# Performance work log

Hardware: AMD Instinct MI355X
Metric: run time of the kernel (lower is better)

The kernel has to match this reference:

```python
import jax, jax.numpy as jnp
import numpy as np

BINS = 10
LOSS_WEIGHT = 1.0
EDGE_TOP = 1.0 + 1e-6  # edges[-1] += 1e-6 in the torch module


def setup_inputs() -> dict:
    key = jax.random.key(0)
    k1, k2, k3 = jax.random.split(key, 3)
    shape = (32, 1048576)
    # pred: sigmoid probabilities in [0, 1)
    pred = jax.random.uniform(k1, shape, dtype=jnp.float32)
    target = (jax.random.uniform(k2, shape) < 0.3).astype(jnp.float32)
    label_weight = (jax.random.uniform(k3, shape) < 0.95).astype(jnp.float32)
    return {"pred": pred, "target": target, "label_weight": label_weight}


def reference(pred, target, label_weight):
    p = pred.reshape(-1)
    t = target.reshape(-1).astype(p.dtype)
    lw = label_weight.reshape(-1).astype(p.dtype)

    I = jnp.sum(p * t)                       # intersection
    S = jnp.sum(p) + jnp.sum(t)              # denominator of Dice

    # gradient norm proxy: |2I/S * pred.detach() - target| (no grad flows through g)
    g = jax.lax.stop_gradient(jnp.abs(2.0 * I / S * p - t))

    valid = lw > 0
    tot = jnp.maximum(jnp.sum(valid.astype(p.dtype)), 1.0)

    # bin assignment: edges are i/bins for i=0..bins, with edges[-1] bumped by 1e-6,
    # so g in [i/bins, (i+1)/bins) -> bin i, and g in [1, 1+1e-6) -> bin bins-1.
    in_range = valid & (g < EDGE_TOP)
    bin_idx = jnp.clip(jnp.floor(g * BINS).astype(jnp.int32), 0, BINS - 1)

    # one-pass histogram of valid, in-range elements
    counts = jnp.zeros(BINS, dtype=p.dtype).at[bin_idx].add(in_range.astype(p.dtype))
    n_nonempty = jnp.sum(counts > 0).astype(p.dtype)

    # weight = tot / num_in_bin for elements in a non-empty bin, else 0; then /n
    per_elem = jnp.where(in_range, tot / jnp.maximum(counts[bin_idx], 1.0), 0.0)
    weights = per_elem / jnp.maximum(n_nonempty, 1.0)

    loss = 1.0 - jnp.sum(2.0 * p * t * weights) / S
    return loss * LOSS_WEIGHT
```

## Files before the change

### kernel.cpp

```cpp
#include <hip/hip_runtime.h>


constexpr int BINS   = 10;
constexpr int K      = 4;
constexpr int CH     = 256 * K;
constexpr int BLOCKS = 2048;
constexpr int OFF1   = 64;
constexpr int OFF2   = 16448;

__global__ __launch_bounds__(256) void k_reduce1(const float4* __restrict__ p,
                                                 const float4* __restrict__ t,
                                                 float* __restrict__ ws,
                                                 int n4, int n) {
    const int tid   = threadIdx.x;
    const int nfull = n4 / CH;
    float sI = 0.f, sP = 0.f, sT = 0.f;

    for (int c = blockIdx.x; c < nfull; c += gridDim.x) {
        const int base = c * CH + tid;
        float4 pv[K], tv[K];
#pragma unroll
        for (int k = 0; k < K; ++k) pv[k] = p[base + k * 256];
#pragma unroll
        for (int k = 0; k < K; ++k) tv[k] = t[base + k * 256];
#pragma unroll
        for (int k = 0; k < K; ++k) {
            sI += pv[k].x * tv[k].x + pv[k].y * tv[k].y + pv[k].z * tv[k].z + pv[k].w * tv[k].w;
            sP += pv[k].x + pv[k].y + pv[k].z + pv[k].w;
            sT += tv[k].x + tv[k].y + tv[k].z + tv[k].w;
        }
    }
    if (blockIdx.x == 0) {
        for (int i = nfull * CH + tid; i < n4; i += 256) {
            float4 pv = p[i], tv = t[i];
            sI += pv.x * tv.x + pv.y * tv.y + pv.z * tv.z + pv.w * tv.w;
            sP += pv.x + pv.y + pv.z + pv.w;
            sT += tv.x + tv.y + tv.z + tv.w;
        }
        if (tid == 0) {
            const float* pf = (const float*)p;
            const float* tf = (const float*)t;
            for (int i = n4 * 4; i < n; ++i) { sI += pf[i] * tf[i]; sP += pf[i]; sT += tf[i]; }
        }
    }
#pragma unroll
    for (int o = 32; o > 0; o >>= 1) {
        sI += __shfl_down(sI, o);
        sP += __shfl_down(sP, o);
        sT += __shfl_down(sT, o);
    }
    __shared__ float rI[4], rP[4], rT[4];
    int wave = tid >> 6, lane = tid & 63;
    if (lane == 0) { rI[wave] = sI; rP[wave] = sP; rT[wave] = sT; }
    __syncthreads();
    if (tid == 0) {
        float* o = &ws[OFF1 + blockIdx.x * 4];
        o[0] = rI[0] + rI[1] + rI[2] + rI[3];
        o[1] = rP[0] + rP[1] + rP[2] + rP[3];
        o[2] = rT[0] + rT[1] + rT[2] + rT[3];
    }
}

__global__ __launch_bounds__(256) void k_mid(float* __restrict__ ws, int nb1) {
    const float4* pws = (const float4*)&ws[OFF1];
    float aI = 0.f, aP = 0.f, aT = 0.f;
    for (int b = threadIdx.x; b < nb1; b += 256) {
        float4 v = pws[b];
        aI += v.x; aP += v.y; aT += v.z;
    }
    __shared__ float red[256 * 5];
    float* mine = &red[threadIdx.x * 5];
    mine[0] = aI; mine[1] = aP; mine[2] = aT;
    __syncthreads();
    int tid = threadIdx.x;
    if (tid < 3) {
        float s = 0.f;
        for (int i = 0; i < 256; ++i) s += red[i * 5 + tid];
        red[tid] = s;
    }
    __syncthreads();
    if (tid == 0) {
        float I = red[0];
        float S = red[1] + red[2];
        ws[0] = 2.f * I / S;
        ws[1] = S;
    }
}

__global__ __launch_bounds__(256) void k_pass2(const float4* __restrict__ p,
                                               const float4* __restrict__ t,
                                               const float4* __restrict__ lw,
                                               float* __restrict__ ws,
                                               int n4, int n) {
    const float scale    = ws[0];
    const float edge_top = 1.0f + 1e-6f;
    const int tid   = threadIdx.x;
    const int nfull = n4 / CH;

    int   cnt[BINS];
    float sm[BINS];
#pragma unroll
    for (int b = 0; b < BINS; ++b) { cnt[b] = 0; sm[b] = 0.f; }
    int vcount = 0;

    auto process = [&](float pe, float te, float we) {
        bool valid = we > 0.f;
        vcount += valid;
        float g = fabsf(scale * pe - te);
        bool inr = valid && (g < edge_top);
        int b = (int)(g * 10.f);
        b = b > (BINS - 1) ? (BINS - 1) : b;
        int slot = inr ? b : BINS;
        float adds = 2.f * pe * te;
#pragma unroll
        for (int b0 = 0; b0 < BINS; ++b0) {
            bool m = (slot == b0);
            cnt[b0] += m;
            sm[b0]  += m ? adds : 0.f;
        }
    };

    for (int c = blockIdx.x; c < nfull; c += gridDim.x) {
        const int base = c * CH + tid;
        float4 pv[K], tv[K], wv[K];
#pragma unroll
        for (int k = 0; k < K; ++k) pv[k] = p[base + k * 256];
#pragma unroll
        for (int k = 0; k < K; ++k) tv[k] = t[base + k * 256];
#pragma unroll
        for (int k = 0; k < K; ++k) wv[k] = lw[base + k * 256];
#pragma unroll
        for (int k = 0; k < K; ++k) {
            process(pv[k].x, tv[k].x, wv[k].x);
            process(pv[k].y, tv[k].y, wv[k].y);
            process(pv[k].z, tv[k].z, wv[k].z);
            process(pv[k].w, tv[k].w, wv[k].w);
        }
    }
    if (blockIdx.x == 0) {
        for (int i = nfull * CH + tid; i < n4; i += 256) {
            float4 pv = p[i], tv = t[i], wv = lw[i];
            process(pv.x, tv.x, wv.x);
            process(pv.y, tv.y, wv.y);
            process(pv.z, tv.z, wv.z);
            process(pv.w, tv.w, wv.w);
        }
        if (tid == 0) {
            const float* pf = (const float*)p;
            const float* tf = (const float*)t;
            const float* wf = (const float*)lw;
            for (int i = n4 * 4; i < n; ++i) process(pf[i], tf[i], wf[i]);
        }
    }

    __shared__ float red[256 * 21];
    float* mine = &red[tid * 21];
#pragma unroll
    for (int b0 = 0; b0 < BINS; ++b0) {
        mine[b0]        = (float)cnt[b0];
        mine[BINS + b0] = sm[b0];
    }
    mine[2 * BINS] = (float)vcount;
    __syncthreads();

    if (tid < 2 * BINS + 1) {
        float v = 0.f;
        for (int i = 0; i < 256; ++i) v += red[i * 21 + tid];
        ws[OFF2 + blockIdx.x * 24 + tid] = v;
    }
}

__global__ __launch_bounds__(256) void k_final(const float* __restrict__ ws,
                                               float* __restrict__ out, int nb2) {
    float acc[24];
#pragma unroll
    for (int s = 0; s < 24; ++s) acc[s] = 0.f;

    for (int b = threadIdx.x; b < nb2; b += 256) {
        const float4* rec = (const float4*)&ws[OFF2 + b * 24];
        float4 v0 = rec[0], v1 = rec[1], v2 = rec[2],
               v3 = rec[3], v4 = rec[4], v5 = rec[5];
        acc[0]  += v0.x; acc[1]  += v0.y; acc[2]  += v0.z; acc[3]  += v0.w;
        acc[4]  += v1.x; acc[5]  += v1.y; acc[6]  += v1.z; acc[7]  += v1.w;
        acc[8]  += v2.x; acc[9]  += v2.y; acc[10] += v2.z; acc[11] += v2.w;
        acc[12] += v3.x; acc[13] += v3.y; acc[14] += v3.z; acc[15] += v3.w;
        acc[16] += v4.x; acc[17] += v4.y; acc[18] += v4.z; acc[19] += v4.w;
        acc[20] += v5.x;
    }

    __shared__ float red[256 * 25];
    float* mine = &red[threadIdx.x * 25];
#pragma unroll
    for (int s = 0; s <= 2 * BINS; ++s) mine[s] = acc[s];
    __syncthreads();

    __shared__ float fin[24];
    int tid = threadIdx.x;
    if (tid <= 2 * BINS) {
        float s = 0.f;
        for (int i = 0; i < 256; ++i) s += red[i * 25 + tid];
        fin[tid] = s;
    }
    __syncthreads();
    if (tid == 0) {
        float S   = ws[1];
        float tot = fmaxf(fin[20], 1.0f);
        int nne = 0;
        for (int b = 0; b < BINS; ++b) nne += (fin[b] > 0.f) ? 1 : 0;
        float nn = fmaxf((float)nne, 1.0f);
        float wsum = 0.f;
        for (int b = 0; b < BINS; ++b) {
            float c = fmaxf(fin[b], 1.0f);
            wsum += fin[BINS + b] * (tot / c);
        }
        wsum /= nn;
        out[0] = 1.0f - wsum / S;
    }
}

extern "C" void kernel_launch(void* const* d_in, const int* in_sizes, int n_in,
                              void* d_out, int out_size, void* d_ws, size_t ws_size,
                              hipStream_t stream) {
    const float* p  = (const float*)d_in[0];
    const float* t  = (const float*)d_in[1];
    const float* lw = (const float*)d_in[2];
    float* ws  = (float*)d_ws;
    float* out = (float*)d_out;
    int n  = in_sizes[0];
    int n4 = n >> 2;

    k_reduce1<<<BLOCKS, 256, 0, stream>>>((const float4*)p, (const float4*)t, ws, n4, n);
    k_mid<<<1, 256, 0, stream>>>(ws, BLOCKS);
    k_pass2<<<BLOCKS, 256, 0, stream>>>((const float4*)p, (const float4*)t,
                                        (const float4*)lw, ws, n4, n);
    k_final<<<1, 256, 0, stream>>>(ws, out, BLOCKS);
}
```

Before: 401.5 us.

## Pack target and validity bits into a byte mask during pass one

The first reduction pass now also reads label_weight and writes one byte per four elements, holding the nonzero bits of target and label_weight. The histogram pass then reads only pred and this compact mask, so it no longer re-reads the full target and weight arrays. The intent is to cut total HBM traffic across the two passes. In exchange, the mask treats target as strictly binary and tests weights with != 0 instead of > 0. A fallback path is used when the workspace is too small.

```diff
diff --git a/kernel.cpp b/kernel.cpp
--- a/kernel.cpp
+++ b/kernel.cpp
@@ -7,27 +7,47 @@
 constexpr int BLOCKS = 2048;
 constexpr int OFF1   = 64;
 constexpr int OFF2   = 16448;
-
-__global__ __launch_bounds__(256) void k_reduce1(const float4* __restrict__ p,
-                                                 const float4* __restrict__ t,
-                                                 float* __restrict__ ws,
-                                                 int n4, int n) {
+constexpr size_t MASK_OFF = 266240;
+
+template<bool MASK>
+__global__ __launch_bounds__(256) void k_pass1(const float4* __restrict__ p,
+                                               const float4* __restrict__ t,
+                                               const float4* __restrict__ lw,
+                                               unsigned char* __restrict__ mask,
+                                               float* __restrict__ ws,
+                                               int n4, int n) {
     const int tid   = threadIdx.x;
     const int nfull = n4 / CH;
     float sI = 0.f, sP = 0.f, sT = 0.f;
 
     for (int c = blockIdx.x; c < nfull; c += gridDim.x) {
         const int base = c * CH + tid;
-        float4 pv[K], tv[K];
+        float4 pv[K], tv[K], wv[K];
 #pragma unroll
         for (int k = 0; k < K; ++k) pv[k] = p[base + k * 256];
 #pragma unroll
         for (int k = 0; k < K; ++k) tv[k] = t[base + k * 256];
+        if constexpr (MASK) {
+#pragma unroll
+            for (int k = 0; k < K; ++k) wv[k] = lw[base + k * 256];
+        }
 #pragma unroll
         for (int k = 0; k < K; ++k) {
             sI += pv[k].x * tv[k].x + pv[k].y * tv[k].y + pv[k].z * tv[k].z + pv[k].w * tv[k].w;
             sP += pv[k].x + pv[k].y + pv[k].z + pv[k].w;
             sT += tv[k].x + tv[k].y + tv[k].z + tv[k].w;
+            if constexpr (MASK) {
+                unsigned int mb = 0;
+                mb |= (tv[k].x != 0.f) ? 1u   : 0u;
+                mb |= (tv[k].y != 0.f) ? 2u   : 0u;
+                mb |= (tv[k].z != 0.f) ? 4u   : 0u;
+                mb |= (tv[k].w != 0.f) ? 8u   : 0u;
+                mb |= (wv[k].x != 0.f) ? 16u  : 0u;
+                mb |= (wv[k].y != 0.f) ? 32u  : 0u;
+                mb |= (wv[k].z != 0.f) ? 64u  : 0u;
+                mb |= (wv[k].w != 0.f) ? 128u : 0u;
+                mask[base + k * 256] = (unsigned char)mb;
+            }
         }
     }
     if (blockIdx.x == 0) {
@@ -36,6 +56,19 @@
             sI += pv.x * tv.x + pv.y * tv.y + pv.z * tv.z + pv.w * tv.w;
             sP += pv.x + pv.y + pv.z + pv.w;
             sT += tv.x + tv.y + tv.z + tv.w;
+            if constexpr (MASK) {
+                float4 wv = lw[i];
+                unsigned int mb = 0;
+                mb |= (tv.x != 0.f) ? 1u   : 0u;
+                mb |= (tv.y != 0.f) ? 2u   : 0u;
+                mb |= (tv.z != 0.f) ? 4u   : 0u;
+                mb |= (tv.w != 0.f) ? 8u   : 0u;
+                mb |= (wv.x != 0.f) ? 16u  : 0u;
+                mb |= (wv.y != 0.f) ? 32u  : 0u;
+                mb |= (wv.z != 0.f) ? 64u  : 0u;
+                mb |= (wv.w != 0.f) ? 128u : 0u;
+                mask[i] = (unsigned char)mb;
+            }
         }
         if (tid == 0) {
             const float* pf = (const float*)p;
@@ -87,9 +120,11 @@
     }
 }
 
+template<bool MASK>
 __global__ __launch_bounds__(256) void k_pass2(const float4* __restrict__ p,
                                                const float4* __restrict__ t,
                                                const float4* __restrict__ lw,
+                                               const unsigned char* __restrict__ mask,
                                                float* __restrict__ ws,
                                                int n4, int n) {
     const float scale    = ws[0];
@@ -103,8 +138,7 @@
     for (int b = 0; b < BINS; ++b) { cnt[b] = 0; sm[b] = 0.f; }
     int vcount = 0;
 
-    auto process = [&](float pe, float te, float we) {
-        bool valid = we > 0.f;
+    auto process = [&](float pe, float te, bool valid) {
         vcount += valid;
         float g = fabsf(scale * pe - te);
         bool inr = valid && (g < edge_top);
@@ -122,34 +156,49 @@
 
     for (int c = blockIdx.x; c < nfull; c += gridDim.x) {
         const int base = c * CH + tid;
-        float4 pv[K], tv[K], wv[K];
+        float4 pv[K];
 #pragma unroll
         for (int k = 0; k < K; ++k) pv[k] = p[base + k * 256];
-#pragma unroll
-        for (int k = 0; k < K; ++k) tv[k] = t[base + k * 256];
-#pragma unroll
-        for (int k = 0; k < K; ++k) wv[k] = lw[base + k * 256];
-#pragma unroll
-        for (int k = 0; k < K; ++k) {
-            process(pv[k].x, tv[k].x, wv[k].x);
-            process(pv[k].y, tv[k].y, wv[k].y);
-            process(pv[k].z, tv[k].z, wv[k].z);
-            process(pv[k].w, tv[k].w, wv[k].w);
+        if constexpr (MASK) {
+            unsigned char mv[K];
+#pragma unroll
+            for (int k = 0; k < K; ++k) mv[k] = mask[base + k * 256];
+#pragma unroll
+            for (int k = 0; k < K; ++k) {
+                unsigned int m = mv[k];
+                process(pv[k].x, (m & 1u)   ? 1.f : 0.f, (m & 16u)  != 0);
+                process(pv[k].y, (m & 2u)   ? 1.f : 0.f, (m & 32u)  != 0);
+                process(pv[k].z, (m & 4u)   ? 1.f : 0.f, (m & 64u)  != 0);
+                process(pv[k].w, (m & 8u)   ? 1.f : 0.f, (m & 128u) != 0);
+            }
+        } else {
+            float4 tv[K], wv[K];
+#pragma unroll
+            for (int k = 0; k < K; ++k) tv[k] = t[base + k * 256];
+#pragma unroll
+            for (int k = 0; k < K; ++k) wv[k] = lw[base + k * 256];
+#pragma unroll
+            for (int k = 0; k < K; ++k) {
+                process(pv[k].x, tv[k].x, wv[k].x > 0.f);
+                process(pv[k].y, tv[k].y, wv[k].y > 0.f);
+                process(pv[k].z, tv[k].z, wv[k].z > 0.f);
+                process(pv[k].w, tv[k].w, wv[k].w > 0.f);
+            }
         }
     }
     if (blockIdx.x == 0) {
         for (int i = nfull * CH + tid; i < n4; i += 256) {
             float4 pv = p[i], tv = t[i], wv = lw[i];
-            process(pv.x, tv.x, wv.x);
-            process(pv.y, tv.y, wv.y);
-            process(pv.z, tv.z, wv.z);
-            process(pv.w, tv.w, wv.w);
+            process(pv.x, tv.x, wv.x > 0.f);
+            process(pv.y, tv.y, wv.y > 0.f);
+            process(pv.z, tv.z, wv.z > 0.f);
+            process(pv.w, tv.w, wv.w > 0.f);
         }
         if (tid == 0) {
             const float* pf = (const float*)p;
             const float* tf = (const float*)t;
             const float* wf = (const float*)lw;
-            for (int i = n4 * 4; i < n; ++i) process(pf[i], tf[i], wf[i]);
+            for (int i = n4 * 4; i < n; ++i) process(pf[i], tf[i], wf[i] > 0.f);
         }
     }
 
@@ -229,9 +278,22 @@
     int n  = in_sizes[0];
     int n4 = n >> 2;
 
-    k_reduce1<<<BLOCKS, 256, 0, stream>>>((const float4*)p, (const float4*)t, ws, n4, n);
-    k_mid<<<1, 256, 0, stream>>>(ws, BLOCKS);
-    k_pass2<<<BLOCKS, 256, 0, stream>>>((const float4*)p, (const float4*)t,
-                                        (const float4*)lw, ws, n4, n);
-    k_final<<<1, 256, 0, stream>>>(ws, out, BLOCKS);
-}
+    unsigned char* mask = (unsigned char*)d_ws + MASK_OFF;
+    const bool use_mask = ws_size >= MASK_OFF + (size_t)n4;
+
+    if (use_mask) {
+        k_pass1<true><<<BLOCKS, 256, 0, stream>>>((const float4*)p, (const float4*)t,
+                                                  (const float4*)lw, mask, ws, n4, n);
+        k_mid<<<1, 256, 0, stream>>>(ws, BLOCKS);
+        k_pass2<true><<<BLOCKS, 256, 0, stream>>>((const float4*)p, (const float4*)t,
+                                                  (const float4*)lw, mask, ws, n4, n);
+        k_final<<<1, 256, 0, stream>>>(ws, out, BLOCKS);
+    } else {
+        k_pass1<false><<<BLOCKS, 256, 0, stream>>>((const float4*)p, (const float4*)t,
+                                                   (const float4*)lw, mask, ws, n4, n);
+        k_mid<<<1, 256, 0, stream>>>(ws, BLOCKS);
+        k_pass2<false><<<BLOCKS, 256, 0, stream>>>((const float4*)p, (const float4*)t,
+                                                   (const float4*)lw, mask, ws, n4, n);
+        k_final<<<1, 256, 0, stream>>>(ws, out, BLOCKS);
+    }
+}
```

After: 410.0 us. 2.1% more time.
